# Optimization experiments

Measured on AMD Instinct MI355X. Metric: run time of the kernel, lower is better.

Reference implementation:

```python
import jax, jax.numpy as jnp
import numpy as np

B, T, D_MODEL = 2, 2048, 2048
D_HEAD = 128
H_PER_G = 4
N_GROUPS = D_MODEL // (H_PER_G * D_HEAD)  # 4
ROT_BASE = 10000
EPS = 1e-6


def setup_inputs() -> dict:
    key = jax.random.key(0)
    ks = jax.random.split(key, 5)
    s = D_MODEL ** -0.5
    return {
        "x": jax.random.normal(ks[0], (B, T, D_MODEL), jnp.float32),
        "wq": jax.random.normal(ks[1], (D_MODEL, D_MODEL), jnp.float32) * s,
        "wk": jax.random.normal(ks[2], (D_MODEL, D_MODEL // H_PER_G), jnp.float32) * s,
        "wv": jax.random.normal(ks[3], (D_MODEL, D_MODEL // H_PER_G), jnp.float32) * s,
        "wo": jax.random.normal(ks[4], (D_MODEL, D_MODEL), jnp.float32) * s,
        "gq": jnp.ones((N_GROUPS, H_PER_G, D_HEAD), jnp.float32),
        "gk": jnp.ones((N_GROUPS, D_HEAD), jnp.float32),
    }


def _rmsnorm(t):
    rms = jnp.sqrt(jnp.mean(jnp.square(t), axis=-1, keepdims=True) + EPS)
    return t / rms


def _rope(t):
    # t: [..., length, width]
    length, width = t.shape[-2], t.shape[-1]
    pos = jnp.arange(length)[:, None]                       # [t,1]
    dims = jnp.arange(width // 2)[None, :]                  # [1,d/2]
    ang = jnp.power(float(ROT_BASE), -dims / (width // 2))
    rad = (pos * ang).astype(t.dtype)                       # [t,d/2]
    cos, sin = jnp.cos(rad), jnp.sin(rad)
    even, odd = jnp.split(t, 2, axis=-1)
    return jnp.concatenate([even * cos - odd * sin, even * sin + odd * cos], axis=-1)


def reference(x, wq, wk, wv, wo, gq, gk):
    b, t, _ = x.shape
    q = jnp.einsum('bti,io->bto', x, wq)
    k = jnp.einsum('bti,io->bto', x, wk)
    v = jnp.einsum('bti,io->bto', x, wv)
    # b t (g h d) -> b g h t d ; b t (g d) -> b g t d
    q = q.reshape(b, t, N_GROUPS, H_PER_G, D_HEAD).transpose(0, 2, 3, 1, 4)
    k = k.reshape(b, t, N_GROUPS, D_HEAD).transpose(0, 2, 1, 3)
    v = v.reshape(b, t, N_GROUPS, D_HEAD).transpose(0, 2, 1, 3)
    # QK RMSNorm with gains
    q = _rmsnorm(q) * gq[None, :, :, None, :]
    k = _rmsnorm(k) * gk[None, :, None, :]
    # RoPE
    q = _rope(q)
    k = _rope(k)
    mult = jnp.asarray(D_HEAD ** -0.25, x.dtype)
    s = jnp.einsum('bghid,bgjd->bghij', q * mult, k * mult)
    # causal mask: subtract 1e30 where i < j
    i = jnp.arange(t)[:, None]
    j = jnp.arange(t)[None, :]
    s = s - jnp.asarray(1e30, s.dtype) * (i < j)
    p = jax.nn.softmax(s, axis=-1)
    o = jnp.einsum('bghij,bgjd->bghid', p, v)
    o = o.transpose(0, 3, 1, 2, 4).reshape(b, t, D_MODEL)
    return jnp.einsum('bti,io->bto', o, wo)
```

## Files before the change

### kernel.cpp

```cpp
#include <hip/hip_runtime.h>
#include <cstdint>

typedef unsigned short u16;
typedef __attribute__((ext_vector_type(8))) __bf16 bf16x8;
typedef __attribute__((ext_vector_type(4))) float f32x4;
typedef __attribute__((ext_vector_type(8))) unsigned short u16x8;

#define DEV __device__ __forceinline__

DEV u16 f2bf(float f) {
  __bf16 b = (__bf16)f;
  return __builtin_bit_cast(u16, b);
}
DEV float bf2f(u16 h) { return __uint_as_float(((unsigned)h) << 16); }
DEV float exp2_fast(float x) { float r; asm("v_exp_f32 %0, %1" : "=v"(r) : "v"(x)); return r; }
DEV void barrier_mem() { asm volatile("s_barrier" ::: "memory"); }

typedef __attribute__((address_space(1))) void gvoid_t;
typedef __attribute__((address_space(3))) void lvoid_t;

DEV void gload_lds16(const void* g, void* l) {
  __builtin_amdgcn_global_load_lds((gvoid_t*)(void*)(uintptr_t)g,
                                   (lvoid_t*)l, 16, 0, 0);
}

#define B_   2
#define T_   2048
#define DM   2048
#define MROWS (B_*T_)

__global__ void k_convert(const float* __restrict__ in, u16* __restrict__ out, int n4) {
  int i = blockIdx.x * blockDim.x + threadIdx.x;
  if (i >= n4) return;
  float4 v = ((const float4*)in)[i];
  ((ushort4*)out)[i] = make_ushort4(f2bf(v.x), f2bf(v.y), f2bf(v.z), f2bf(v.w));
}

__global__ void k_transpose(const float* __restrict__ in, u16* __restrict__ out, int R, int C) {
  __shared__ float tile[32][33];
  int c0 = blockIdx.x * 32, r0 = blockIdx.y * 32;
  int tx = threadIdx.x, ty = threadIdx.y;
  #pragma unroll
  for (int j = 0; j < 32; j += 8)
    tile[ty + j][tx] = in[(size_t)(r0 + ty + j) * C + c0 + tx];
  __syncthreads();
  #pragma unroll
  for (int j = 0; j < 32; j += 8)
    out[(size_t)(c0 + ty + j) * R + r0 + tx] = f2bf(tile[tx][ty + j]);
}

__global__ void k_rope_table(float2* __restrict__ tab) {
  int i = blockIdx.x * blockDim.x + threadIdx.x;
  int pos = i >> 6, d = i & 63;
  float ang = powf(10000.0f, -(float)d / 64.0f);
  float s, c;
  sincosf((float)pos * ang, &s, &c);
  tab[i] = make_float2(c, s);
}

template <typename OutT>
__global__ __launch_bounds__(256) void k_gemm(
    const u16* __restrict__ A, const u16* __restrict__ BT, OutT* __restrict__ C,
    int M, int N, int K) {
  __shared__ u16 As[128 * 64];
  __shared__ u16 Bs[128 * 64];
  const int tid = threadIdx.x;
  const int w = tid >> 6, lane = tid & 63;
  const int lr = lane & 15, lg = lane >> 4;
  const int m0 = blockIdx.y * 128, n0 = blockIdx.x * 128;
  const int wr = w >> 1, wc = w & 1;
  f32x4 acc[4][4] = {};
  for (int k0 = 0; k0 < K; k0 += 64) {
    __syncthreads();
    #pragma unroll
    for (int i = 0; i < 4; i++) {
      int idx = i * 256 + tid;
      int row = idx >> 3, blk = idx & 7;
      int scol = ((blk ^ (row & 7)) << 3);
      gload_lds16(&A[(size_t)(m0 + row) * K + k0 + scol], &As[(idx & ~63) * 8]);
      gload_lds16(&BT[(size_t)(n0 + row) * K + k0 + scol], &Bs[(idx & ~63) * 8]);
    }
    __syncthreads();
    #pragma unroll
    for (int kk = 0; kk < 2; kk++) {
      bf16x8 af[4], bfr[4];
      #pragma unroll
      for (int m = 0; m < 4; m++) {
        int row = wr * 64 + m * 16 + lr;
        af[m] = *(const bf16x8*)&As[row * 64 + (((kk * 4 + lg) ^ (lr & 7)) << 3)];
      }
      #pragma unroll
      for (int n = 0; n < 4; n++) {
        int row = wc * 64 + n * 16 + lr;
        bfr[n] = *(const bf16x8*)&Bs[row * 64 + (((kk * 4 + lg) ^ (lr & 7)) << 3)];
      }
      #pragma unroll
      for (int m = 0; m < 4; m++)
        #pragma unroll
        for (int n = 0; n < 4; n++)
          acc[m][n] = __builtin_amdgcn_mfma_f32_16x16x32_bf16(af[m], bfr[n], acc[m][n], 0, 0, 0);
    }
  }
  #pragma unroll
  for (int m = 0; m < 4; m++)
    #pragma unroll
    for (int n = 0; n < 4; n++)
      #pragma unroll
      for (int r = 0; r < 4; r++) {
        int row = m0 + wr * 64 + m * 16 + lg * 4 + r;
        int col = n0 + wc * 64 + n * 16 + lr;
        if constexpr (sizeof(OutT) == 2) C[(size_t)row * N + col] = f2bf(acc[m][n][r]);
        else                             C[(size_t)row * N + col] = acc[m][n][r];
      }
}

__global__ void k_norm_rope_q(const u16* __restrict__ qkvf, const float* __restrict__ gq,
                              const float2* __restrict__ tab, u16* __restrict__ qb) {
  int w = threadIdx.x >> 6, lane = threadIdx.x & 63;
  int W = blockIdx.x * 4 + w;
  int h = W & 3, g = (W >> 2) & 3;
  int bt = W >> 4;
  int t = bt & 2047, b = bt >> 11;
  const u16* row = qkvf + (size_t)bt * 3072 + (size_t)(g * 4 + h) * 128;
  float v0 = bf2f(row[lane]);
  float v1 = bf2f(row[lane + 64]);
  float ss = v0 * v0 + v1 * v1;
  #pragma unroll
  for (int off = 1; off < 64; off <<= 1) ss += __shfl_xor(ss, off, 64);
  float inv = 1.0f / sqrtf(ss * (1.0f / 128.0f) + 1e-6f);
  v0 *= inv * gq[(g * 4 + h) * 128 + lane];
  v1 *= inv * gq[(g * 4 + h) * 128 + 64 + lane];
  float2 cs = tab[t * 64 + lane];
  const float sc = 0.1275174f;
  float o0 = (v0 * cs.x - v1 * cs.y) * sc;
  float o1 = (v0 * cs.y + v1 * cs.x) * sc;
  u16* orow = qb + ((size_t)(((b * 4 + g) * 4 + h) * 2048 + t)) * 128;
  orow[lane] = f2bf(o0);
  orow[lane + 64] = f2bf(o1);
}

__global__ void k_norm_rope_k(const u16* __restrict__ qkvf, const float* __restrict__ gk,
                              const float2* __restrict__ tab, u16* __restrict__ kb) {
  int w = threadIdx.x >> 6, lane = threadIdx.x & 63;
  int W = blockIdx.x * 4 + w;
  int g = W & 3;
  int bt = W >> 2;
  int t = bt & 2047, b = bt >> 11;
  const u16* row = qkvf + (size_t)bt * 3072 + 2048 + (size_t)g * 128;
  float v0 = bf2f(row[lane]);
  float v1 = bf2f(row[lane + 64]);
  float ss = v0 * v0 + v1 * v1;
  #pragma unroll
  for (int off = 1; off < 64; off <<= 1) ss += __shfl_xor(ss, off, 64);
  float inv = 1.0f / sqrtf(ss * (1.0f / 128.0f) + 1e-6f);
  v0 *= inv * gk[g * 128 + lane];
  v1 *= inv * gk[g * 128 + 64 + lane];
  float2 cs = tab[t * 64 + lane];
  float o0 = v0 * cs.x - v1 * cs.y;
  float o1 = v0 * cs.y + v1 * cs.x;
  u16* orow = kb + ((size_t)((b * 4 + g) * 2048 + t)) * 128;
  orow[lane] = f2bf(o0);
  orow[lane + 64] = f2bf(o1);
}

__global__ void k_pack_vt(const u16* __restrict__ qkvf, u16* __restrict__ vt) {
  int w = threadIdx.x >> 6, lane = threadIdx.x & 63;
  int W = blockIdx.x * 4 + w;
  int t8 = W & 255, dh = (W >> 8) & 1, bg = W >> 9;
  int b = bg >> 2, g = bg & 3;
  int t0 = t8 * 8;
  int d = dh * 64 + lane;
  u16x8 pack;
  #pragma unroll
  for (int j = 0; j < 8; j++)
    pack[j] = qkvf[(size_t)(b * 2048 + t0 + j) * 3072 + 2560 + g * 128 + d];
  *(u16x8*)&vt[((size_t)(bg * 128 + d)) * 2048 + t0] = pack;
}

DEV void stage_tiles(const u16* kh, const u16* vh, int j0, u16* Kbuf, u16* Vbuf, int tid) {
  #pragma unroll
  for (int i = 0; i < 4; i++) {
    int idx = i * 256 + tid;
    int row = idx >> 4, blk = idx & 15;
    gload_lds16(&kh[(size_t)(j0 + row) * 128 + ((blk ^ (row & 7)) << 3)],
                &Kbuf[(idx & ~63) * 8]);
  }
  #pragma unroll
  for (int i = 0; i < 4; i++) {
    int idx = i * 256 + tid;
    int row = idx >> 3, blk = idx & 7;
    gload_lds16(&vh[(size_t)row * T_ + j0 + ((blk ^ (row & 7)) << 3)],
                &Vbuf[(idx & ~63) * 8]);
  }
}

DEV void attn_tile(const u16* __restrict__ Kc, const u16* __restrict__ Vc,
                   u16* __restrict__ Psw, const bf16x8* qf, f32x4* oacc,
                   float& lsum, int lr, int lg, int w, bool diag) {
  f32x4 s[4] = {};
  __builtin_amdgcn_s_setprio(1);
  #pragma unroll
  for (int kk = 0; kk < 4; kk++) {
    #pragma unroll
    for (int c = 0; c < 4; c++) {
      const int kvr = c * 16 + lr;
      bf16x8 kf = *(const bf16x8*)&Kc[kvr * 128 + (((kk * 4 + lg) ^ (kvr & 7)) << 3)];
      s[c] = __builtin_amdgcn_mfma_f32_16x16x32_bf16(kf, qf[kk], s[c], 0, 0, 0);
    }
  }
  __builtin_amdgcn_s_setprio(0);
  if (diag) {
    #pragma unroll
    for (int c = 0; c < 4; c++)
      #pragma unroll
      for (int r = 0; r < 4; r++)
        if (c * 16 + lg * 4 + r > w * 16 + lr) s[c][r] = -1.0e30f;
  }
  float rs = 0.f;
  #pragma unroll
  for (int c = 0; c < 4; c++)
    #pragma unroll
    for (int r = 0; r < 4; r++) {
      float pv = exp2_fast(s[c][r]);
      s[c][r] = pv;
      rs += pv;
    }
  lsum += rs;
  #pragma unroll
  for (int c = 0; c < 4; c++) {
    ushort4 q4 = make_ushort4(f2bf(s[c][0]), f2bf(s[c][1]), f2bf(s[c][2]), f2bf(s[c][3]));
    int blk8 = (c * 4 + lg) ^ ((lr & 7) << 1);
    *(ushort4*)&Psw[lr * 64 + blk8 * 4] = q4;
  }
  #pragma unroll
  for (int ks = 0; ks < 2; ks++) {
    bf16x8 pf = *(const bf16x8*)&Psw[lr * 64 +
                 (((2 * (ks * 4 + lg)) ^ ((lr & 7) << 1)) << 2)];
    __builtin_amdgcn_s_setprio(1);
    #pragma unroll
    for (int nd = 0; nd < 8; nd++) {
      const int d = nd * 16 + lr;
      bf16x8 vf = *(const bf16x8*)&Vc[d * 64 + (((ks * 4 + lg) ^ (d & 7)) << 3)];
      oacc[nd] = __builtin_amdgcn_mfma_f32_16x16x32_bf16(pf, vf, oacc[nd], 0, 0, 0);
    }
    __builtin_amdgcn_s_setprio(0);
  }
}

DEV void attn_epilogue(u16* __restrict__ ob, int b, int g, int h, int q0,
                       const f32x4* oacc, float lsum, int lr, int lg, int w) {
  lsum += __shfl_xor(lsum, 16, 64);
  lsum += __shfl_xor(lsum, 32, 64);
  float inv = 1.0f / lsum;
  float iv[4];
  #pragma unroll
  for (int r = 0; r < 4; r++) iv[r] = __shfl(inv, lg * 4 + r, 64);
  #pragma unroll
  for (int r = 0; r < 4; r++) {
    int orow = q0 + w * 16 + lg * 4 + r;
    size_t base = (size_t)(b * T_ + orow) * 2048 + (size_t)(g * 4 + h) * 128;
    #pragma unroll
    for (int nd = 0; nd < 8; nd++)
      ob[base + nd * 16 + lr] = f2bf(oacc[nd][r] * iv[r]);
  }
}

__global__ __launch_bounds__(256) void k_attn(
    const u16* __restrict__ qb, const u16* __restrict__ kb,
    const u16* __restrict__ vtb, u16* __restrict__ ob) {
  __shared__ __align__(16) u16 Ks[2][64 * 128];
  __shared__ __align__(16) u16 Vs[2][128 * 64];
  __shared__ __align__(16) u16 Ps[4][16 * 64];
  const int bid = blockIdx.x;
  const int hg = bid & 7;
  const int rest = bid >> 3;
  const int hh = rest & 3;
  const int p = rest >> 2;
  const int head = hg * 4 + hh;
  const int b = hg >> 2, g = hg & 3, h = hh;
  const int tid = threadIdx.x;
  const int w = tid >> 6, lane = tid & 63;
  const int lr = lane & 15, lg = lane >> 4;
  const u16* qh = qb + (size_t)head * (T_ * 128);
  const u16* kh = kb + (size_t)hg * (T_ * 128);
  const u16* vh = vtb + (size_t)hg * (128 * T_);

  #pragma unroll 1
  for (int half = 0; half < 2; ++half) {
    const int qblk = half ? p : 31 - p;
    const int q0 = qblk * 64;
    bf16x8 qf[4];
    const int qrow = q0 + w * 16 + lr;
    #pragma unroll
    for (int kk = 0; kk < 4; kk++)
      qf[kk] = *(const bf16x8*)&qh[(size_t)qrow * 128 + kk * 32 + lg * 8];

    f32x4 oacc[8] = {};
    float lsum = 0.f;

    stage_tiles(kh, vh, 0, Ks[0], Vs[0], tid);
    asm volatile("s_waitcnt vmcnt(0)" ::: "memory");
    barrier_mem();
    int cur = 0;
    for (int jt = 0; jt <= qblk; ++jt) {
      if (jt < qblk)
        stage_tiles(kh, vh, (jt + 1) * 64, Ks[cur ^ 1], Vs[cur ^ 1], tid);
      attn_tile(Ks[cur], Vs[cur], Ps[w], qf, oacc, lsum, lr, lg, w, jt == qblk);
      asm volatile("s_waitcnt vmcnt(0)" ::: "memory");
      barrier_mem();
      cur ^= 1;
    }
    attn_epilogue(ob, b, g, h, q0, oacc, lsum, lr, lg, w);
  }
}

#define OFF_XB    ((size_t)0)
#define OFF_WQKVT ((size_t)16777216)
#define OFF_WOT   ((size_t)29360128)
#define OFF_ROPE  ((size_t)37748736)
#define OFF_QB    ((size_t)38797312)
#define OFF_KB    ((size_t)55574528)
#define OFF_VTB   ((size_t)59768832)
#define OFF_QKVF  ((size_t)63963136)
#define OFF_OB    OFF_QKVF

extern "C" void kernel_launch(void* const* d_in, const int* in_sizes, int n_in,
                              void* d_out, int out_size, void* d_ws, size_t ws_size,
                              hipStream_t stream) {
  const float* x  = (const float*)d_in[0];
  const float* wq = (const float*)d_in[1];
  const float* wk = (const float*)d_in[2];
  const float* wv = (const float*)d_in[3];
  const float* wo = (const float*)d_in[4];
  const float* gq = (const float*)d_in[5];
  const float* gk = (const float*)d_in[6];
  float* out = (float*)d_out;
  char* ws = (char*)d_ws;

  u16*    xb    = (u16*)(ws + OFF_XB);
  u16*    wqkvt = (u16*)(ws + OFF_WQKVT);
  u16*    wot   = (u16*)(ws + OFF_WOT);
  float2* rope  = (float2*)(ws + OFF_ROPE);
  u16*    qbuf  = (u16*)(ws + OFF_QB);
  u16*    kbuf  = (u16*)(ws + OFF_KB);
  u16*    vtb   = (u16*)(ws + OFF_VTB);
  u16*    qkvf  = (u16*)(ws + OFF_QKVF);
  u16*    obuf  = (u16*)(ws + OFF_OB);

  k_convert<<<8192, 256, 0, stream>>>(x, xb, (MROWS * DM) / 4);
  k_transpose<<<dim3(64, 64), dim3(32, 8), 0, stream>>>(wq, wqkvt, 2048, 2048);
  k_transpose<<<dim3(16, 64), dim3(32, 8), 0, stream>>>(wk, wqkvt + (size_t)2048 * 2048, 2048, 512);
  k_transpose<<<dim3(16, 64), dim3(32, 8), 0, stream>>>(wv, wqkvt + (size_t)2560 * 2048, 2048, 512);
  k_transpose<<<dim3(64, 64), dim3(32, 8), 0, stream>>>(wo, wot, 2048, 2048);
  k_rope_table<<<512, 256, 0, stream>>>(rope);
  k_gemm<u16><<<dim3(24, 32), 256, 0, stream>>>(xb, wqkvt, qkvf, MROWS, 3072, 2048);
  k_norm_rope_q<<<16384, 256, 0, stream>>>(qkvf, gq, rope, qbuf);
  k_norm_rope_k<<<4096, 256, 0, stream>>>(qkvf, gk, rope, kbuf);
  k_pack_vt<<<1024, 256, 0, stream>>>(qkvf, vtb);
  k_attn<<<512, 256, 0, stream>>>(qbuf, kbuf, vtb, obuf);
  k_gemm<float><<<dim3(16, 32), 256, 0, stream>>>(obuf, wot, out, MROWS, 2048, 2048);
}
```

Baseline: 215.5 us.

## Fuse Q norm/RoPE into attention, merge prep kernels, swizzle GEMM block order

The weight transposes and rope table are merged into one k_prep launch, and the K norm/RoPE and V transpose share one k_postgemm launch. The Q RMSNorm+RoPE now runs inside the attention kernel straight from the QKV GEMM output, which removes the separate Q buffer write and read. The GEMM remaps block indices in strides of eight, likely to improve L2 reuse across XCDs. This cuts launch overhead and memory traffic, but each attention block recomputes Q normalization for both of its halves and adds register pressure in the prologue.

```diff
diff --git a/kernel.cpp b/kernel.cpp
--- a/kernel.cpp
+++ b/kernel.cpp
@@ -28,6 +28,7 @@
 #define T_   2048
 #define DM   2048
 #define MROWS (B_*T_)
+#define QSC  0.1275174f
 
 __global__ void k_convert(const float* __restrict__ in, u16* __restrict__ out, int n4) {
   int i = blockIdx.x * blockDim.x + threadIdx.x;
@@ -36,26 +37,38 @@
   ((ushort4*)out)[i] = make_ushort4(f2bf(v.x), f2bf(v.y), f2bf(v.z), f2bf(v.w));
 }
 
-__global__ void k_transpose(const float* __restrict__ in, u16* __restrict__ out, int R, int C) {
+__global__ void k_prep(const float* __restrict__ wq, const float* __restrict__ wk,
+                       const float* __restrict__ wv, const float* __restrict__ wo,
+                       u16* __restrict__ wqkvt, u16* __restrict__ wot,
+                       float2* __restrict__ rope) {
+  const int bid = blockIdx.x;
+  const int tid = threadIdx.x;
+  if (bid >= 10240) {
+    int i = (bid - 10240) * 256 + tid;
+    int pos = i >> 6, d = i & 63;
+    float ang = powf(10000.0f, -(float)d / 64.0f);
+    float s, c;
+    sincosf((float)pos * ang, &s, &c);
+    rope[i] = make_float2(c, s);
+    return;
+  }
   __shared__ float tile[32][33];
-  int c0 = blockIdx.x * 32, r0 = blockIdx.y * 32;
-  int tx = threadIdx.x, ty = threadIdx.y;
+  const float* in;
+  u16* out;
+  int C, bx, by, crow0;
+  if (bid < 4096)      { in = wq; out = wqkvt; C = 2048; bx = bid & 63;          by = bid >> 6;          crow0 = 0; }
+  else if (bid < 5120) { in = wk; out = wqkvt; C = 512;  bx = (bid - 4096) & 15; by = (bid - 4096) >> 4; crow0 = 2048; }
+  else if (bid < 6144) { in = wv; out = wqkvt; C = 512;  bx = (bid - 5120) & 15; by = (bid - 5120) >> 4; crow0 = 2560; }
+  else                 { in = wo; out = wot;   C = 2048; bx = (bid - 6144) & 63; by = (bid - 6144) >> 6; crow0 = 0; }
+  const int c0 = bx * 32, r0 = by * 32;
+  const int tx = tid & 31, ty = tid >> 5;
   #pragma unroll
   for (int j = 0; j < 32; j += 8)
     tile[ty + j][tx] = in[(size_t)(r0 + ty + j) * C + c0 + tx];
   __syncthreads();
   #pragma unroll
   for (int j = 0; j < 32; j += 8)
-    out[(size_t)(c0 + ty + j) * R + r0 + tx] = f2bf(tile[tx][ty + j]);
-}
-
-__global__ void k_rope_table(float2* __restrict__ tab) {
-  int i = blockIdx.x * blockDim.x + threadIdx.x;
-  int pos = i >> 6, d = i & 63;
-  float ang = powf(10000.0f, -(float)d / 64.0f);
-  float s, c;
-  sincosf((float)pos * ang, &s, &c);
-  tab[i] = make_float2(c, s);
+    out[(size_t)(crow0 + c0 + ty + j) * 2048 + r0 + tx] = f2bf(tile[tx][ty + j]);
 }
 
 template <typename OutT>
@@ -67,7 +80,11 @@
   const int tid = threadIdx.x;
   const int w = tid >> 6, lane = tid & 63;
   const int lr = lane & 15, lg = lane >> 4;
-  const int m0 = blockIdx.y * 128, n0 = blockIdx.x * 128;
+  const int nx = gridDim.x;
+  const int flat = blockIdx.y * nx + blockIdx.x;
+  const int cpx = (nx * gridDim.y) >> 3;
+  const int f = (flat & 7) * cpx + (flat >> 3);
+  const int m0 = (f / nx) * 128, n0 = (f % nx) * 128;
   const int wr = w >> 1, wc = w & 1;
   f32x4 acc[4][4] = {};
   for (int k0 = 0; k0 < K; k0 += 64) {
@@ -114,67 +131,43 @@
       }
 }
 
-__global__ void k_norm_rope_q(const u16* __restrict__ qkvf, const float* __restrict__ gq,
-                              const float2* __restrict__ tab, u16* __restrict__ qb) {
-  int w = threadIdx.x >> 6, lane = threadIdx.x & 63;
-  int W = blockIdx.x * 4 + w;
-  int h = W & 3, g = (W >> 2) & 3;
-  int bt = W >> 4;
-  int t = bt & 2047, b = bt >> 11;
-  const u16* row = qkvf + (size_t)bt * 3072 + (size_t)(g * 4 + h) * 128;
-  float v0 = bf2f(row[lane]);
-  float v1 = bf2f(row[lane + 64]);
-  float ss = v0 * v0 + v1 * v1;
-  #pragma unroll
-  for (int off = 1; off < 64; off <<= 1) ss += __shfl_xor(ss, off, 64);
-  float inv = 1.0f / sqrtf(ss * (1.0f / 128.0f) + 1e-6f);
-  v0 *= inv * gq[(g * 4 + h) * 128 + lane];
-  v1 *= inv * gq[(g * 4 + h) * 128 + 64 + lane];
-  float2 cs = tab[t * 64 + lane];
-  const float sc = 0.1275174f;
-  float o0 = (v0 * cs.x - v1 * cs.y) * sc;
-  float o1 = (v0 * cs.y + v1 * cs.x) * sc;
-  u16* orow = qb + ((size_t)(((b * 4 + g) * 4 + h) * 2048 + t)) * 128;
-  orow[lane] = f2bf(o0);
-  orow[lane + 64] = f2bf(o1);
-}
-
-__global__ void k_norm_rope_k(const u16* __restrict__ qkvf, const float* __restrict__ gk,
-                              const float2* __restrict__ tab, u16* __restrict__ kb) {
-  int w = threadIdx.x >> 6, lane = threadIdx.x & 63;
-  int W = blockIdx.x * 4 + w;
-  int g = W & 3;
-  int bt = W >> 2;
-  int t = bt & 2047, b = bt >> 11;
-  const u16* row = qkvf + (size_t)bt * 3072 + 2048 + (size_t)g * 128;
-  float v0 = bf2f(row[lane]);
-  float v1 = bf2f(row[lane + 64]);
-  float ss = v0 * v0 + v1 * v1;
-  #pragma unroll
-  for (int off = 1; off < 64; off <<= 1) ss += __shfl_xor(ss, off, 64);
-  float inv = 1.0f / sqrtf(ss * (1.0f / 128.0f) + 1e-6f);
-  v0 *= inv * gk[g * 128 + lane];
-  v1 *= inv * gk[g * 128 + 64 + lane];
-  float2 cs = tab[t * 64 + lane];
-  float o0 = v0 * cs.x - v1 * cs.y;
-  float o1 = v0 * cs.y + v1 * cs.x;
-  u16* orow = kb + ((size_t)((b * 4 + g) * 2048 + t)) * 128;
-  orow[lane] = f2bf(o0);
-  orow[lane + 64] = f2bf(o1);
-}
-
-__global__ void k_pack_vt(const u16* __restrict__ qkvf, u16* __restrict__ vt) {
-  int w = threadIdx.x >> 6, lane = threadIdx.x & 63;
-  int W = blockIdx.x * 4 + w;
-  int t8 = W & 255, dh = (W >> 8) & 1, bg = W >> 9;
-  int b = bg >> 2, g = bg & 3;
-  int t0 = t8 * 8;
-  int d = dh * 64 + lane;
-  u16x8 pack;
-  #pragma unroll
-  for (int j = 0; j < 8; j++)
-    pack[j] = qkvf[(size_t)(b * 2048 + t0 + j) * 3072 + 2560 + g * 128 + d];
-  *(u16x8*)&vt[((size_t)(bg * 128 + d)) * 2048 + t0] = pack;
+__global__ void k_postgemm(const u16* __restrict__ qkvf, const float* __restrict__ gk,
+                           const float2* __restrict__ tab, u16* __restrict__ kb,
+                           u16* __restrict__ vt) {
+  const int bid = blockIdx.x;
+  const int w = threadIdx.x >> 6, lane = threadIdx.x & 63;
+  if (bid < 4096) {
+    int W = bid * 4 + w;
+    int g = W & 3;
+    int bt = W >> 2;
+    int t = bt & 2047, b = bt >> 11;
+    const u16* row = qkvf + (size_t)bt * 3072 + 2048 + (size_t)g * 128;
+    float v0 = bf2f(row[lane]);
+    float v1 = bf2f(row[lane + 64]);
+    float ss = v0 * v0 + v1 * v1;
+    #pragma unroll
+    for (int off = 1; off < 64; off <<= 1) ss += __shfl_xor(ss, off, 64);
+    float inv = 1.0f / sqrtf(ss * (1.0f / 128.0f) + 1e-6f);
+    v0 *= inv * gk[g * 128 + lane];
+    v1 *= inv * gk[g * 128 + 64 + lane];
+    float2 cs = tab[t * 64 + lane];
+    float o0 = v0 * cs.x - v1 * cs.y;
+    float o1 = v0 * cs.y + v1 * cs.x;
+    u16* orow = kb + ((size_t)((b * 4 + g) * 2048 + t)) * 128;
+    orow[lane] = f2bf(o0);
+    orow[lane + 64] = f2bf(o1);
+  } else {
+    int W = (bid - 4096) * 4 + w;
+    int t8 = W & 255, dh = (W >> 8) & 1, bg = W >> 9;
+    int b = bg >> 2, g = bg & 3;
+    int t0 = t8 * 8;
+    int d = dh * 64 + lane;
+    u16x8 pack;
+    #pragma unroll
+    for (int j = 0; j < 8; j++)
+      pack[j] = qkvf[(size_t)(b * 2048 + t0 + j) * 3072 + 2560 + g * 128 + d];
+    *(u16x8*)&vt[((size_t)(bg * 128 + d)) * 2048 + t0] = pack;
+  }
 }
 
 DEV void stage_tiles(const u16* kh, const u16* vh, int j0, u16* Kbuf, u16* Vbuf, int tid) {
@@ -266,7 +259,8 @@
 }
 
 __global__ __launch_bounds__(256) void k_attn(
-    const u16* __restrict__ qb, const u16* __restrict__ kb,
+    const u16* __restrict__ qkvf, const float* __restrict__ gq,
+    const float2* __restrict__ rope, const u16* __restrict__ kb,
     const u16* __restrict__ vtb, u16* __restrict__ ob) {
   __shared__ __align__(16) u16 Ks[2][64 * 128];
   __shared__ __align__(16) u16 Vs[2][128 * 64];
@@ -276,24 +270,54 @@
   const int rest = bid >> 3;
   const int hh = rest & 3;
   const int p = rest >> 2;
-  const int head = hg * 4 + hh;
   const int b = hg >> 2, g = hg & 3, h = hh;
   const int tid = threadIdx.x;
   const int w = tid >> 6, lane = tid & 63;
   const int lr = lane & 15, lg = lane >> 4;
-  const u16* qh = qb + (size_t)head * (T_ * 128);
   const u16* kh = kb + (size_t)hg * (T_ * 128);
   const u16* vh = vtb + (size_t)hg * (128 * T_);
+  const float* gqh = gq + (size_t)(g * 4 + h) * 128;
 
   #pragma unroll 1
   for (int half = 0; half < 2; ++half) {
     const int qblk = half ? p : 31 - p;
     const int q0 = qblk * 64;
     bf16x8 qf[4];
-    const int qrow = q0 + w * 16 + lr;
-    #pragma unroll
-    for (int kk = 0; kk < 4; kk++)
-      qf[kk] = *(const bf16x8*)&qh[(size_t)qrow * 128 + kk * 32 + lg * 8];
+    {
+      const int qrow = q0 + w * 16 + lr;
+      const u16* qsrc = qkvf + (size_t)(b * T_ + qrow) * 3072 + (size_t)(g * 4 + h) * 128;
+      float qe[4][8];
+      float ss = 0.f;
+      #pragma unroll
+      for (int kk = 0; kk < 4; kk++) {
+        u16x8 raw = *(const u16x8*)&qsrc[kk * 32 + lg * 8];
+        #pragma unroll
+        for (int j = 0; j < 8; j++) {
+          float v = bf2f(raw[j]);
+          qe[kk][j] = v;
+          ss += v * v;
+        }
+      }
+      ss += __shfl_xor(ss, 16, 64);
+      ss += __shfl_xor(ss, 32, 64);
+      float inv = 1.0f / sqrtf(ss * (1.0f / 128.0f) + 1e-6f);
+      #pragma unroll
+      for (int kk = 0; kk < 2; kk++) {
+        const float2* tp = &rope[(size_t)qrow * 64 + kk * 32 + lg * 8];
+        u16x8 lo, hi;
+        #pragma unroll
+        for (int j = 0; j < 8; j++) {
+          int d = kk * 32 + lg * 8 + j;
+          float v0 = qe[kk][j] * inv * gqh[d];
+          float v1 = qe[kk + 2][j] * inv * gqh[d + 64];
+          float2 cs = tp[j];
+          lo[j] = f2bf((v0 * cs.x - v1 * cs.y) * QSC);
+          hi[j] = f2bf((v0 * cs.y + v1 * cs.x) * QSC);
+        }
+        qf[kk] = __builtin_bit_cast(bf16x8, lo);
+        qf[kk + 2] = __builtin_bit_cast(bf16x8, hi);
+      }
+    }
 
     f32x4 oacc[8] = {};
     float lsum = 0.f;
@@ -318,11 +342,10 @@
 #define OFF_WQKVT ((size_t)16777216)
 #define OFF_WOT   ((size_t)29360128)
 #define OFF_ROPE  ((size_t)37748736)
-#define OFF_QB    ((size_t)38797312)
+#define OFF_OB    ((size_t)38797312)
 #define OFF_KB    ((size_t)55574528)
 #define OFF_VTB   ((size_t)59768832)
 #define OFF_QKVF  ((size_t)63963136)
-#define OFF_OB    OFF_QKVF
 
 extern "C" void kernel_launch(void* const* d_in, const int* in_sizes, int n_in,
                               void* d_out, int out_size, void* d_ws, size_t ws_size,
@@ -341,22 +364,15 @@
   u16*    wqkvt = (u16*)(ws + OFF_WQKVT);
   u16*    wot   = (u16*)(ws + OFF_WOT);
   float2* rope  = (float2*)(ws + OFF_ROPE);
-  u16*    qbuf  = (u16*)(ws + OFF_QB);
+  u16*    obuf  = (u16*)(ws + OFF_OB);
   u16*    kbuf  = (u16*)(ws + OFF_KB);
   u16*    vtb   = (u16*)(ws + OFF_VTB);
   u16*    qkvf  = (u16*)(ws + OFF_QKVF);
-  u16*    obuf  = (u16*)(ws + OFF_OB);
 
   k_convert<<<8192, 256, 0, stream>>>(x, xb, (MROWS * DM) / 4);
-  k_transpose<<<dim3(64, 64), dim3(32, 8), 0, stream>>>(wq, wqkvt, 2048, 2048);
-  k_transpose<<<dim3(16, 64), dim3(32, 8), 0, stream>>>(wk, wqkvt + (size_t)2048 * 2048, 2048, 512);
-  k_transpose<<<dim3(16, 64), dim3(32, 8), 0, stream>>>(wv, wqkvt + (size_t)2560 * 2048, 2048, 512);
-  k_transpose<<<dim3(64, 64), dim3(32, 8), 0, stream>>>(wo, wot, 2048, 2048);
-  k_rope_table<<<512, 256, 0, stream>>>(rope);
+  k_prep<<<10752, 256, 0, stream>>>(wq, wk, wv, wo, wqkvt, wot, rope);
   k_gemm<u16><<<dim3(24, 32), 256, 0, stream>>>(xb, wqkvt, qkvf, MROWS, 3072, 2048);
-  k_norm_rope_q<<<16384, 256, 0, stream>>>(qkvf, gq, rope, qbuf);
-  k_norm_rope_k<<<4096, 256, 0, stream>>>(qkvf, gk, rope, kbuf);
-  k_pack_vt<<<1024, 256, 0, stream>>>(qkvf, vtb);
-  k_attn<<<512, 256, 0, stream>>>(qbuf, kbuf, vtb, obuf);
+  k_postgemm<<<5120, 256, 0, stream>>>(qkvf, gk, rope, kbuf, vtb);
+  k_attn<<<512, 256, 0, stream>>>(qkvf, gq, rope, kbuf, vtb, obuf);
   k_gemm<float><<<dim3(16, 32), 256, 0, stream>>>(obuf, wot, out, MROWS, 2048, 2048);
 }
```

After: 199.2 us. 1.08x faster.
